# Performance work log

Measured on AMD Instinct MI355X. Metric: run time of the kernel, lower is better.

## Reference

```python
import jax, jax.numpy as jnp
import numpy as np

TAU = 2.0      # spikingjelly LIFNode default tau
V_TH = 1.0     # default v_threshold
ALPHA = 4.0    # default surrogate.Sigmoid alpha
H, HL = 8, 2   # num_heads, local_heads

@jax.custom_vjp
def spike(u):
    # Heaviside: fire when membrane potential >= threshold (u = v - v_th)
    return (u >= 0.0).astype(u.dtype)

def _spike_fwd(u):
    return spike(u), u

def _spike_bwd(u, g):
    s = jax.nn.sigmoid(ALPHA * u)
    return (g * ALPHA * s * (1.0 - s),)

spike.defvjp(_spike_fwd, _spike_bwd)

def lif(x):
    # Multi-step LIF, decay_input=False, v_reset=0.0 (hard reset), detach_reset=True.
    # Charge: v = v - (v - 0)/tau + x ; spike when v >= v_th ; reset v -> 0 where spiked.
    decay = 1.0 - 1.0 / TAU
    def step(v, xt):
        v = v * decay + xt
        s = spike(v - V_TH)
        v = v * (1.0 - jax.lax.stop_gradient(s))  # detach_reset
        return v, s
    _, spikes = jax.lax.scan(step, jnp.zeros_like(x[0]), x)
    return spikes

def setup_inputs() -> dict:
    key = jax.random.key(0)
    ks = jax.random.split(key, 5)
    T, B, C, D = 4, 8, 512, 768
    hd = D // H            # 96
    mkv = hd * HL          # 192 (GQA kv projection width)
    scale = 0.1            # keeps LIF membrane potentials near threshold
    return {
        "x": jax.random.normal(ks[0], (T, B, C, D), jnp.float32),
        "q_w": jax.random.normal(ks[1], (D, D), jnp.float32) * scale,
        "k_w": jax.random.normal(ks[2], (mkv, D), jnp.float32) * scale,
        "v_w": jax.random.normal(ks[3], (mkv, D), jnp.float32) * scale,
        "wo_w": jax.random.normal(ks[4], (D, D), jnp.float32) * scale,
    }

def reference(x, q_w, k_w, v_w, wo_w):
    T, B, C, D = x.shape
    hd = D // H
    n_rep = H // HL
    xs = lif(x)  # proj_lif
    # q: (T,B,C,D) -> (T,B,H,C,hd)
    q = lif(xs @ q_w.T).reshape(T, B, C, H, hd).transpose(0, 1, 3, 2, 4)
    # k,v: (T,B,C,mkv) -> repeat_interleave over kv heads -> (T,B,H,C,hd)
    k = lif(xs @ k_w.T).reshape(T, B, C, HL, hd)
    k = jnp.repeat(k, n_rep, axis=3).transpose(0, 1, 3, 2, 4)
    v = lif(xs @ v_w.T).reshape(T, B, C, HL, hd)
    v = jnp.repeat(v, n_rep, axis=3).transpose(0, 1, 3, 2, 4)
    # softmax-free attention: (q k^T) * 0.1 @ v
    scores = jnp.einsum('tbhqd,tbhkd->tbhqk', q, k) * 0.1
    out = jnp.einsum('tbhqk,tbhkd->tbhqd', scores, v)
    # (T,B,H,C,hd) -> (T,B,C,D)
    out = out.transpose(0, 1, 3, 2, 4).reshape(T, B, C, D)
    return out @ wo_w.T
```

## Files before the change

kernel.cpp:

```cpp
#include <hip/hip_runtime.h>

typedef __bf16 bf16;
typedef __bf16 bf16x8 __attribute__((ext_vector_type(8)));
typedef float f32x4 __attribute__((ext_vector_type(4)));

#define T_ 4
#define B_ 8
#define C_ 512
#define D_ 768
#define H_ 8
#define HL_ 2
#define HD_ 96
#define MKV_ 192
#define M2_ 4096
#define BCD_ 3145728
#define M3_ 16384
#define NCOMB 1152
#define SUSP_CAP 65536
#define SUSP_WIN 2e-4f

__device__ __forceinline__ void gld16(const bf16* g, bf16* l) {
    __builtin_amdgcn_global_load_lds(
        (const __attribute__((address_space(1))) unsigned int*)g,
        (__attribute__((address_space(3))) unsigned int*)l, 16, 0, 0);
}

__global__ __launch_bounds__(256) void prep_kernel(
    const float* __restrict__ x, const float* __restrict__ q_w,
    const float* __restrict__ k_w, const float* __restrict__ v_w,
    const float* __restrict__ wo_w, bf16* __restrict__ xs,
    bf16* __restrict__ whi, bf16* __restrict__ wlo, bf16* __restrict__ wo_bf,
    unsigned* __restrict__ susp)
{
    const int t0 = blockIdx.x * 256 + threadIdx.x;
    const int stride = gridDim.x * 256;
    if (t0 == 0) susp[0] = 0;
    for (int i = t0; i < BCD_; i += stride) {
        double v = 0.0;
        #pragma unroll
        for (int t = 0; t < T_; ++t) {
            v = v * 0.5 + (double)x[(size_t)t * BCD_ + i];
            float s = (v >= 1.0) ? 1.0f : 0.0f;
            xs[(size_t)t * BCD_ + i] = (bf16)s;
            if (s != 0.0f) v = 0.0;
        }
    }
    for (int i = t0; i < NCOMB * D_; i += stride) {
        int row = i / D_, col = i - row * D_;
        float v;
        if (row < 768)      v = q_w[(size_t)row * D_ + col];
        else if (row < 960) v = k_w[(size_t)(row - 768) * D_ + col];
        else                v = v_w[(size_t)(row - 960) * D_ + col];
        bf16 h = (bf16)v;
        whi[i] = h;
        wlo[i] = (bf16)(v - (float)h);
    }
    for (int i = t0; i < D_ * D_; i += stride)
        wo_bf[i] = (bf16)wo_w[i];
}

__global__ __launch_bounds__(256, 3) void proj_lif_kernel(
    const bf16* __restrict__ xs, const bf16* __restrict__ Whi,
    const bf16* __restrict__ Wlo,
    bf16* __restrict__ q_sp, bf16* __restrict__ k_sp, bf16* __restrict__ v_sp,
    unsigned* __restrict__ susp)
{
    __shared__ __align__(16) bf16 A0[T_][64 * 32];
    __shared__ __align__(16) bf16 A1[T_][64 * 32];
    __shared__ __align__(16) bf16 H0[64 * 32];
    __shared__ __align__(16) bf16 H1[64 * 32];
    __shared__ __align__(16) bf16 L0[64 * 32];
    __shared__ __align__(16) bf16 L1[64 * 32];

    const int tid  = threadIdx.x;
    const int wave = tid >> 6, lane = tid & 63;
    const int m16  = lane & 15, quad = lane >> 4;
    const int wm   = wave >> 1, wn = wave & 1;

    const int bid   = blockIdx.y * 64 + blockIdx.x;
    const int xcd   = bid & 7;
    const int local = bid >> 3;
    const int m0    = ((xcd << 3) | (local & 7)) * 64;
    const int n0    = (local >> 3) * 64;

    const int colb = n0 + wn * 32;
    bf16* outp; int Nloc, cb;
    if (colb < 768)      { outp = q_sp; Nloc = 768; cb = colb; }
    else if (colb < 960) { outp = k_sp; Nloc = 192; cb = colb - 768; }
    else                 { outp = v_sp; Nloc = 192; cb = colb - 960; }

    f32x4 acc[T_][2][2];
    #pragma unroll
    for (int t = 0; t < T_; t++)
        #pragma unroll
        for (int a = 0; a < 2; a++)
            #pragma unroll
            for (int b = 0; b < 2; b++) { f32x4 z = {0.f,0.f,0.f,0.f}; acc[t][a][b] = z; }

    const int srow = tid >> 2;
    const int sseg = (tid & 3) ^ ((tid >> 3) & 3);

#define STAGE(Ab, Hb, Lb, k0) do {                                            \
    _Pragma("unroll")                                                         \
    for (int t = 0; t < T_; t++)                                              \
        gld16(xs + (size_t)(t * M2_ + m0 + srow) * D_ + (k0) + sseg * 8,      \
              &Ab[t][tid * 8]);                                               \
    gld16(Whi + (size_t)(n0 + srow) * D_ + (k0) + sseg * 8, &Hb[tid * 8]);    \
    gld16(Wlo + (size_t)(n0 + srow) * D_ + (k0) + sseg * 8, &Lb[tid * 8]);    \
} while (0)

    bf16x8 a[T_][2], bh[2], bl[2];

#define LOADREGS(Ab, Hb, Lb) do {                                             \
    _Pragma("unroll")                                                         \
    for (int mi = 0; mi < 2; mi++) {                                          \
        int row = wm * 32 + mi * 16 + m16;                                    \
        int off = row * 32 + ((quad ^ ((row >> 1) & 3)) * 8);                 \
        _Pragma("unroll")                                                     \
        for (int t = 0; t < T_; t++) a[t][mi] = *(const bf16x8*)&Ab[t][off];  \
    }                                                                         \
    _Pragma("unroll")                                                         \
    for (int ni = 0; ni < 2; ni++) {                                          \
        int row = wn * 32 + ni * 16 + m16;                                    \
        int off = row * 32 + ((quad ^ ((row >> 1) & 3)) * 8);                 \
        bh[ni] = *(const bf16x8*)&Hb[off];                                    \
        bl[ni] = *(const bf16x8*)&Lb[off];                                    \
    }                                                                         \
} while (0)

#define DOMFMA() do {                                                         \
    __builtin_amdgcn_s_setprio(1);                                            \
    _Pragma("unroll")                                                         \
    for (int ni = 0; ni < 2; ni++)                                            \
        _Pragma("unroll")                                                     \
        for (int t = 0; t < T_; t++)                                          \
            _Pragma("unroll")                                                 \
            for (int mi = 0; mi < 2; mi++) {                                  \
                acc[t][mi][ni] = __builtin_amdgcn_mfma_f32_16x16x32_bf16(     \
                    a[t][mi], bh[ni], acc[t][mi][ni], 0, 0, 0);               \
                acc[t][mi][ni] = __builtin_amdgcn_mfma_f32_16x16x32_bf16(     \
                    a[t][mi], bl[ni], acc[t][mi][ni], 0, 0, 0);               \
            }                                                                 \
    __builtin_amdgcn_s_setprio(0);                                            \
} while (0)

#define READS_DONE() do {                                                     \
    asm volatile("s_waitcnt lgkmcnt(0)" ::: "memory");                        \
    __builtin_amdgcn_s_barrier();                                             \
    __builtin_amdgcn_sched_barrier(0);                                        \
} while (0)

#define NEXT_READY(N) do {                                                    \
    asm volatile("s_waitcnt vmcnt(" #N ")" ::: "memory");                     \
    __builtin_amdgcn_s_barrier();                                             \
} while (0)

    STAGE(A0, H0, L0, 0);
    STAGE(A1, H1, L1, 32);
    NEXT_READY(6);

    for (int s = 0; s < 22; s += 2) {
        LOADREGS(A0, H0, L0);
        READS_DONE();
        STAGE(A0, H0, L0, (s + 2) * 32);
        DOMFMA();
        NEXT_READY(6);

        LOADREGS(A1, H1, L1);
        READS_DONE();
        STAGE(A1, H1, L1, (s + 3) * 32);
        DOMFMA();
        NEXT_READY(6);
    }
    LOADREGS(A0, H0, L0);
    READS_DONE();
    DOMFMA();
    NEXT_READY(0);
    LOADREGS(A1, H1, L1);
    DOMFMA();

#undef STAGE
#undef LOADREGS
#undef DOMFMA
#undef READS_DONE
#undef NEXT_READY

    #pragma unroll
    for (int mi = 0; mi < 2; mi++)
        #pragma unroll
        for (int ni = 0; ni < 2; ni++)
            #pragma unroll
            for (int rr = 0; rr < 4; rr++) {
                int row = m0 + wm * 32 + mi * 16 + quad * 4 + rr;
                int lc  = cb + ni * 16 + m16;
                float v = 0.f;
                bool suspect = false;
                #pragma unroll
                for (int t = 0; t < T_; t++) {
                    v = v * 0.5f + acc[t][mi][ni][rr];
                    float d = v - 1.0f;
                    if (fabsf(d) < SUSP_WIN) suspect = true;
                    float sp = (d >= 0.f) ? 1.f : 0.f;
                    v *= (1.f - sp);
                    outp[(size_t)(t * M2_ + row) * Nloc + lc] = (bf16)sp;
                }
                if (suspect) {
                    int ccol = n0 + wn * 32 + ni * 16 + m16;
                    unsigned idx = atomicAdd(susp, 1u);
                    if (idx < SUSP_CAP) susp[1 + idx] = (unsigned)(row * 2048 + ccol);
                }
            }
}

__global__ __launch_bounds__(256) void fixup_kernel(
    const bf16* __restrict__ xs, const float* __restrict__ q_w,
    const float* __restrict__ k_w, const float* __restrict__ v_w,
    bf16* __restrict__ q_sp, bf16* __restrict__ k_sp, bf16* __restrict__ v_sp,
    const unsigned* __restrict__ susp)
{
    unsigned count = susp[0];
    if (count > SUSP_CAP) count = SUSP_CAP;
    const int lane = threadIdx.x & 63;
    const int wid  = (blockIdx.x * blockDim.x + threadIdx.x) >> 6;
    const int nw   = (gridDim.x * blockDim.x) >> 6;
    for (unsigned i = wid; i < count; i += nw) {
        unsigned e = susp[1 + i];
        int row = e >> 11, col = e & 2047;
        const float* W; bf16* outp; int Nloc, lc;
        if (col < 768)      { W = q_w + (size_t)col * D_;         outp = q_sp; Nloc = 768; lc = col; }
        else if (col < 960) { W = k_w + (size_t)(col - 768) * D_; outp = k_sp; Nloc = 192; lc = col - 768; }
        else                { W = v_w + (size_t)(col - 960) * D_; outp = v_sp; Nloc = 192; lc = col - 960; }
        double v = 0.0;
        for (int t = 0; t < T_; ++t) {
            const bf16* ar = xs + (size_t)(t * M2_ + row) * D_;
            double y = 0.0;
            for (int k = lane; k < D_; k += 64)
                y += (double)(float)ar[k] * (double)W[k];
            #pragma unroll
            for (int off = 1; off < 64; off <<= 1)
                y += __shfl_xor(y, off);
            v = v * 0.5 + y;
            unsigned sp = (v >= 1.0) ? 1u : 0u;
            if (lane == 0) outp[(size_t)(t * M2_ + row) * Nloc + lc] = (bf16)(float)sp;
            if (sp) v = 0.0;
        }
    }
}

__global__ __launch_bounds__(256) void ktv_kernel(
    const bf16* __restrict__ k_sp, const bf16* __restrict__ v_sp,
    float* __restrict__ M_part)
{
    const int g    = blockIdx.x;
    const int cc   = blockIdx.y;
    const int kvh  = g % HL_;
    const int tb   = g / HL_;
    const int wave = threadIdx.x >> 6;
    const int lane = threadIdx.x & 63;
    const int m16  = lane & 15, quad = lane >> 4;

    __shared__ __align__(16) bf16 klds[96 * 40];
    __shared__ __align__(16) bf16 vlds[96 * 40];

    f32x4 acc[9];
    #pragma unroll
    for (int i = 0; i < 9; i++) { f32x4 z = {0.f,0.f,0.f,0.f}; acc[i] = z; }

    const bf16* kbase = k_sp + ((size_t)tb * C_ + cc * 64) * MKV_ + kvh * HD_;
    const bf16* vbase = v_sp + ((size_t)tb * C_ + cc * 64) * MKV_ + kvh * HD_;

    for (int c0 = 0; c0 < 64; c0 += 32) {
        __syncthreads();
        for (int ci = threadIdx.x; ci < 768; ci += 256) {
            int arr = ci & 1;
            int pos = ci >> 1;
            int c = pos / 12, seg = pos - c * 12;
            const bf16* src = (arr ? vbase : kbase) + (size_t)(c0 + c) * MKV_ + seg * 8;
            bf16x8 val = *(const bf16x8*)src;
            bf16* dst = arr ? vlds : klds;
            #pragma unroll
            for (int e = 0; e < 8; e++)
                dst[(seg * 8 + e) * 40 + c] = val[e];
        }
        __syncthreads();
        #pragma unroll
        for (int i = 0; i < 9; i++) {
            int tile = wave + i * 4;
            int mt = tile / 6, nt = tile % 6;
            bf16x8 a = *(const bf16x8*)(&klds[(mt * 16 + m16) * 40 + quad * 8]);
            bf16x8 b = *(const bf16x8*)(&vlds[(nt * 16 + m16) * 40 + quad * 8]);
            acc[i] = __builtin_amdgcn_mfma_f32_16x16x32_bf16(a, b, acc[i], 0, 0, 0);
        }
    }
    float* op = M_part + ((size_t)cc * 64 + g) * HD_ * HD_;
    #pragma unroll
    for (int i = 0; i < 9; i++) {
        int tile = wave + i * 4;
        int mt = tile / 6, nt = tile % 6;
        #pragma unroll
        for (int r = 0; r < 4; r++) {
            int d = mt * 16 + quad * 4 + r;
            int j = nt * 16 + m16;
            op[(size_t)j * HD_ + d] = acc[i][r];
        }
    }
}

__global__ __launch_bounds__(256) void cvtM_kernel(
    const float* __restrict__ M_part, bf16* __restrict__ M_hi,
    bf16* __restrict__ M_lo)
{
    int i = blockIdx.x * 256 + threadIdx.x;
    if (i >= 64 * HD_ * HD_) return;
    float m = 0.f;
    #pragma unroll
    for (int j = 0; j < 8; j++)
        m += M_part[i + (size_t)j * 589824];
    bf16 h = (bf16)m;
    M_hi[i] = h;
    M_lo[i] = (bf16)(m - (float)h);
}

__global__ __launch_bounds__(256) void qm_kernel(
    const bf16* __restrict__ q_sp, const bf16* __restrict__ M_hi,
    const bf16* __restrict__ M_lo, bf16* __restrict__ out_attn)
{
    const int tbh  = blockIdx.x;
    const int h    = tbh % H_;
    const int tb   = tbh / H_;
    const int g    = tb * HL_ + (h >> 2);
    const int wave = threadIdx.x >> 6;
    const int lane = threadIdx.x & 63;
    const int m16  = lane & 15, quad = lane >> 4;
    const int cw   = blockIdx.y * 128 + wave * 32;

    __shared__ __align__(16) bf16 Mh[96 * 104];
    __shared__ __align__(16) bf16 Ml[96 * 104];
    {
        const bf16* gh = M_hi + (size_t)g * HD_ * HD_;
        const bf16* gl = M_lo + (size_t)g * HD_ * HD_;
        #pragma unroll
        for (int j = 0; j < 5; j++) {
            int ci = j * 256 + threadIdx.x;
            if (ci < 1152) {
                int row = ci / 12, seg = ci % 12;
                *(bf16x8*)&Mh[row * 104 + seg * 8] = *(const bf16x8*)(gh + row * HD_ + seg * 8);
                *(bf16x8*)&Ml[row * 104 + seg * 8] = *(const bf16x8*)(gl + row * HD_ + seg * 8);
            }
        }
    }
    __syncthreads();

    f32x4 acc[2][6];
    #pragma unroll
    for (int mi = 0; mi < 2; mi++)
        #pragma unroll
        for (int nt = 0; nt < 6; nt++) { f32x4 z = {0.f,0.f,0.f,0.f}; acc[mi][nt] = z; }

    #pragma unroll
    for (int ks = 0; ks < 3; ++ks) {
        bf16x8 a[2];
        #pragma unroll
        for (int mi = 0; mi < 2; mi++)
            a[mi] = *(const bf16x8*)(q_sp + ((size_t)(tb * C_ + cw + mi * 16 + m16)) * D_
                                     + h * HD_ + ks * 32 + quad * 8);
        #pragma unroll
        for (int nt = 0; nt < 6; ++nt) {
            bf16x8 bh = *(const bf16x8*)&Mh[(nt * 16 + m16) * 104 + ks * 32 + quad * 8];
            bf16x8 bl = *(const bf16x8*)&Ml[(nt * 16 + m16) * 104 + ks * 32 + quad * 8];
            #pragma unroll
            for (int mi = 0; mi < 2; mi++) {
                acc[mi][nt] = __builtin_amdgcn_mfma_f32_16x16x32_bf16(a[mi], bh, acc[mi][nt], 0, 0, 0);
                acc[mi][nt] = __builtin_amdgcn_mfma_f32_16x16x32_bf16(a[mi], bl, acc[mi][nt], 0, 0, 0);
            }
        }
    }
    #pragma unroll
    for (int mi = 0; mi < 2; mi++)
        #pragma unroll
        for (int nt = 0; nt < 6; nt++)
            #pragma unroll
            for (int r = 0; r < 4; r++) {
                int c = cw + mi * 16 + quad * 4 + r;
                int j = nt * 16 + m16;
                out_attn[((size_t)(tb * C_ + c)) * D_ + h * HD_ + j] = (bf16)(0.1f * acc[mi][nt][r]);
            }
}

__global__ __launch_bounds__(256) void final_gemm_kernel(
    const bf16* __restrict__ A, const bf16* __restrict__ W, float* __restrict__ out)
{
    __shared__ __align__(16) bf16 Alds[128 * 64];
    __shared__ __align__(16) bf16 Blds[128 * 64];
    const int tid  = threadIdx.x;
    const int wave = tid >> 6, lane = tid & 63;
    const int m16  = lane & 15, quad = lane >> 4;
    const int wm   = wave >> 1, wn = wave & 1;
    const int m0   = blockIdx.x * 128, n0 = blockIdx.y * 128;

    f32x4 acc[4][4];
    #pragma unroll
    for (int a = 0; a < 4; a++)
        #pragma unroll
        for (int b = 0; b < 4; b++) { f32x4 z = {0.f,0.f,0.f,0.f}; acc[a][b] = z; }

    for (int k0 = 0; k0 < D_; k0 += 64) {
        __syncthreads();
        #pragma unroll
        for (int j = 0; j < 4; j++) {
            int ci = j * 256 + tid;
            int row = ci >> 3, slot = ci & 7;
            int seg = slot ^ ((row >> 1) & 7);
            gld16(A + (size_t)(m0 + row) * D_ + k0 + seg * 8, Alds + ci * 8);
            gld16(W + (size_t)(n0 + row) * D_ + k0 + seg * 8, Blds + ci * 8);
        }
        __syncthreads();
        #pragma unroll
        for (int kc = 0; kc < 2; kc++) {
            bf16x8 a[4], b[4];
            #pragma unroll
            for (int mi = 0; mi < 4; mi++) {
                int row = wm * 64 + mi * 16 + m16;
                a[mi] = *(const bf16x8*)&Alds[row * 64 + (((kc * 4 + quad) ^ ((row >> 1) & 7)) * 8)];
            }
            #pragma unroll
            for (int ni = 0; ni < 4; ni++) {
                int row = wn * 64 + ni * 16 + m16;
                b[ni] = *(const bf16x8*)&Blds[row * 64 + (((kc * 4 + quad) ^ ((row >> 1) & 7)) * 8)];
            }
            #pragma unroll
            for (int mi = 0; mi < 4; mi++)
                #pragma unroll
                for (int ni = 0; ni < 4; ni++)
                    acc[mi][ni] = __builtin_amdgcn_mfma_f32_16x16x32_bf16(a[mi], b[ni], acc[mi][ni], 0, 0, 0);
        }
    }
    #pragma unroll
    for (int mi = 0; mi < 4; mi++)
        #pragma unroll
        for (int ni = 0; ni < 4; ni++)
            #pragma unroll
            for (int r = 0; r < 4; r++) {
                int row = m0 + wm * 64 + mi * 16 + quad * 4 + r;
                int col = n0 + wn * 64 + ni * 16 + m16;
                out[(size_t)row * D_ + col] = acc[mi][ni][r];
            }
}

extern "C" void kernel_launch(void* const* d_in, const int* in_sizes, int n_in,
                              void* d_out, int out_size, void* d_ws, size_t ws_size,
                              hipStream_t stream) {
    const float* x    = (const float*)d_in[0];
    const float* q_w  = (const float*)d_in[1];
    const float* k_w  = (const float*)d_in[2];
    const float* v_w  = (const float*)d_in[3];
    const float* wo_w = (const float*)d_in[4];
    float* out = (float*)d_out;

    char* ws = (char*)d_ws;
    bf16* xs    = (bf16*)(ws);
    bf16* q_sp  = (bf16*)(ws + 25165824);
    bf16* k_sp  = (bf16*)(ws + 50331648);
    bf16* v_sp  = (bf16*)(ws + 56623104);
    bf16* whi   = (bf16*)(ws + 62914560);
    bf16* wlo   = (bf16*)(ws + 64684032);
    bf16* wo_bf = (bf16*)(ws + 66453504);
    bf16* M_hi  = (bf16*)(ws + 67633152);
    bf16* M_lo  = (bf16*)(ws + 68812800);
    unsigned* susp = (unsigned*)(ws + 69992448);
    bf16* out_attn = xs;
    float* M_part  = out;

    hipLaunchKernelGGL(prep_kernel, dim3(2048), dim3(256), 0, stream,
                       x, q_w, k_w, v_w, wo_w, xs, whi, wlo, wo_bf, susp);
    hipLaunchKernelGGL(proj_lif_kernel, dim3(M2_ / 64, NCOMB / 64), dim3(256), 0, stream,
                       xs, whi, wlo, q_sp, k_sp, v_sp, susp);
    hipLaunchKernelGGL(fixup_kernel, dim3(256), dim3(256), 0, stream,
                       xs, q_w, k_w, v_w, q_sp, k_sp, v_sp, susp);
    hipLaunchKernelGGL(ktv_kernel, dim3(T_ * B_ * HL_, 8), dim3(256), 0, stream,
                       k_sp, v_sp, M_part);
    hipLaunchKernelGGL(cvtM_kernel, dim3((64 * HD_ * HD_ + 255) / 256), dim3(256), 0, stream,
                       M_part, M_hi, M_lo);
    hipLaunchKernelGGL(qm_kernel, dim3(T_ * B_ * H_, C_ / 128), dim3(256), 0, stream,
                       q_sp, M_hi, M_lo, out_attn);
    hipLaunchKernelGGL(final_gemm_kernel, dim3(M3_ / 128, D_ / 128), dim3(256), 0, stream,
                       out_attn, wo_bf, out);
}
```

Measured before the change: 266.0 us.

## Vectorize prep, fuse fixup into projection epilogue, double-buffer final GEMM

Prep now handles 8 elements of the LIF input scan and 4 elements of each weight conversion per thread, using vector loads and stores. The separate fixup kernel and its global atomic suspect list go away. Each projection wave instead ballots its near-threshold outputs and recomputes them in double precision in its own epilogue, which saves a launch but can serialize waves that hit many suspects. The final GEMM switches to double-buffered 32-wide K stages with explicit waitcnt and barrier pipelining and launch_bounds 3, so loads overlap MFMA work.

New measurement: 255.8 us. 1.04x faster.

```diff
diff --git a/kernel.cpp b/kernel.cpp
--- a/kernel.cpp
+++ b/kernel.cpp
@@ -1,6 +1,7 @@
 #include <hip/hip_runtime.h>
 
 typedef __bf16 bf16;
+typedef __bf16 bf16x4 __attribute__((ext_vector_type(4)));
 typedef __bf16 bf16x8 __attribute__((ext_vector_type(8)));
 typedef float f32x4 __attribute__((ext_vector_type(4)));
 
@@ -16,7 +17,6 @@
 #define BCD_ 3145728
 #define M3_ 16384
 #define NCOMB 1152
-#define SUSP_CAP 65536
 #define SUSP_WIN 2e-4f
 
 __device__ __forceinline__ void gld16(const bf16* g, bf16* l) {
@@ -25,45 +25,76 @@
         (__attribute__((address_space(3))) unsigned int*)l, 16, 0, 0);
 }
 
+#define READS_DONE() do {                                                     \
+    asm volatile("s_waitcnt lgkmcnt(0)" ::: "memory");                        \
+    __builtin_amdgcn_s_barrier();                                             \
+    __builtin_amdgcn_sched_barrier(0);                                        \
+} while (0)
+
+#define NEXT_READY(N) do {                                                    \
+    asm volatile("s_waitcnt vmcnt(" #N ")" ::: "memory");                     \
+    __builtin_amdgcn_s_barrier();                                             \
+} while (0)
+
 __global__ __launch_bounds__(256) void prep_kernel(
     const float* __restrict__ x, const float* __restrict__ q_w,
     const float* __restrict__ k_w, const float* __restrict__ v_w,
     const float* __restrict__ wo_w, bf16* __restrict__ xs,
-    bf16* __restrict__ whi, bf16* __restrict__ wlo, bf16* __restrict__ wo_bf,
-    unsigned* __restrict__ susp)
+    bf16* __restrict__ whi, bf16* __restrict__ wlo, bf16* __restrict__ wo_bf)
 {
     const int t0 = blockIdx.x * 256 + threadIdx.x;
     const int stride = gridDim.x * 256;
-    if (t0 == 0) susp[0] = 0;
-    for (int i = t0; i < BCD_; i += stride) {
-        double v = 0.0;
+    for (int i = t0 * 8; i < BCD_; i += stride * 8) {
+        double v[8] = {0.0, 0.0, 0.0, 0.0, 0.0, 0.0, 0.0, 0.0};
         #pragma unroll
         for (int t = 0; t < T_; ++t) {
-            v = v * 0.5 + (double)x[(size_t)t * BCD_ + i];
-            float s = (v >= 1.0) ? 1.0f : 0.0f;
-            xs[(size_t)t * BCD_ + i] = (bf16)s;
-            if (s != 0.0f) v = 0.0;
-        }
-    }
-    for (int i = t0; i < NCOMB * D_; i += stride) {
+            const float* xp = x + (size_t)t * BCD_ + i;
+            f32x4 xa = *(const f32x4*)xp;
+            f32x4 xb = *(const f32x4*)(xp + 4);
+            bf16x8 s;
+            #pragma unroll
+            for (int e = 0; e < 8; ++e) {
+                float xe = (e < 4) ? xa[e] : xb[e - 4];
+                v[e] = v[e] * 0.5 + (double)xe;
+                float sp = (v[e] >= 1.0) ? 1.f : 0.f;
+                s[e] = (bf16)sp;
+                v[e] *= (double)(1.f - sp);
+            }
+            *(bf16x8*)(xs + (size_t)t * BCD_ + i) = s;
+        }
+    }
+    for (int i = t0 * 4; i < NCOMB * D_; i += stride * 4) {
         int row = i / D_, col = i - row * D_;
-        float v;
-        if (row < 768)      v = q_w[(size_t)row * D_ + col];
-        else if (row < 960) v = k_w[(size_t)(row - 768) * D_ + col];
-        else                v = v_w[(size_t)(row - 960) * D_ + col];
-        bf16 h = (bf16)v;
-        whi[i] = h;
-        wlo[i] = (bf16)(v - (float)h);
-    }
-    for (int i = t0; i < D_ * D_; i += stride)
-        wo_bf[i] = (bf16)wo_w[i];
+        const float* src;
+        if (row < 768)      src = q_w + (size_t)row * D_ + col;
+        else if (row < 960) src = k_w + (size_t)(row - 768) * D_ + col;
+        else                src = v_w + (size_t)(row - 960) * D_ + col;
+        f32x4 wv = *(const f32x4*)src;
+        bf16x4 hh, ll;
+        #pragma unroll
+        for (int e = 0; e < 4; ++e) {
+            bf16 h = (bf16)wv[e];
+            hh[e] = h;
+            ll[e] = (bf16)(wv[e] - (float)h);
+        }
+        *(bf16x4*)(whi + i) = hh;
+        *(bf16x4*)(wlo + i) = ll;
+    }
+    for (int i = t0 * 4; i < D_ * D_; i += stride * 4) {
+        f32x4 wv = *(const f32x4*)(wo_w + i);
+        bf16x4 c;
+        #pragma unroll
+        for (int e = 0; e < 4; ++e) c[e] = (bf16)wv[e];
+        *(bf16x4*)(wo_bf + i) = c;
+    }
 }
 
 __global__ __launch_bounds__(256, 3) void proj_lif_kernel(
     const bf16* __restrict__ xs, const bf16* __restrict__ Whi,
     const bf16* __restrict__ Wlo,
-    bf16* __restrict__ q_sp, bf16* __restrict__ k_sp, bf16* __restrict__ v_sp,
-    unsigned* __restrict__ susp)
+    const float* __restrict__ q_w, const float* __restrict__ k_w,
+    const float* __restrict__ v_w,
+    bf16* __restrict__ q_sp, bf16* __restrict__ k_sp, bf16* __restrict__ v_sp)
 {
     __shared__ __align__(16) bf16 A0[T_][64 * 32];
     __shared__ __align__(16) bf16 A1[T_][64 * 32];
@@ -144,17 +175,6 @@
     __builtin_amdgcn_s_setprio(0);                                            \
 } while (0)
 
-#define READS_DONE() do {                                                     \
-    asm volatile("s_waitcnt lgkmcnt(0)" ::: "memory");                        \
-    __builtin_amdgcn_s_barrier();                                             \
-    __builtin_amdgcn_sched_barrier(0);                                        \
-} while (0)
-
-#define NEXT_READY(N) do {                                                    \
-    asm volatile("s_waitcnt vmcnt(" #N ")" ::: "memory");                     \
-    __builtin_amdgcn_s_barrier();                                             \
-} while (0)
-
     STAGE(A0, H0, L0, 0);
     STAGE(A1, H1, L1, 32);
     NEXT_READY(6);
@@ -182,9 +202,8 @@
 #undef STAGE
 #undef LOADREGS
 #undef DOMFMA
-#undef READS_DONE
-#undef NEXT_READY
-
+
+    unsigned susmask = 0;
     #pragma unroll
     for (int mi = 0; mi < 2; mi++)
         #pragma unroll
@@ -204,45 +223,38 @@
                     v *= (1.f - sp);
                     outp[(size_t)(t * M2_ + row) * Nloc + lc] = (bf16)sp;
                 }
-                if (suspect) {
-                    int ccol = n0 + wn * 32 + ni * 16 + m16;
-                    unsigned idx = atomicAdd(susp, 1u);
-                    if (idx < SUSP_CAP) susp[1 + idx] = (unsigned)(row * 2048 + ccol);
-                }
-            }
-}
-
-__global__ __launch_bounds__(256) void fixup_kernel(
-    const bf16* __restrict__ xs, const float* __restrict__ q_w,
-    const float* __restrict__ k_w, const float* __restrict__ v_w,
-    bf16* __restrict__ q_sp, bf16* __restrict__ k_sp, bf16* __restrict__ v_sp,
-    const unsigned* __restrict__ susp)
-{
-    unsigned count = susp[0];
-    if (count > SUSP_CAP) count = SUSP_CAP;
-    const int lane = threadIdx.x & 63;
-    const int wid  = (blockIdx.x * blockDim.x + threadIdx.x) >> 6;
-    const int nw   = (gridDim.x * blockDim.x) >> 6;
-    for (unsigned i = wid; i < count; i += nw) {
-        unsigned e = susp[1 + i];
-        int row = e >> 11, col = e & 2047;
-        const float* W; bf16* outp; int Nloc, lc;
-        if (col < 768)      { W = q_w + (size_t)col * D_;         outp = q_sp; Nloc = 768; lc = col; }
-        else if (col < 960) { W = k_w + (size_t)(col - 768) * D_; outp = k_sp; Nloc = 192; lc = col - 768; }
-        else                { W = v_w + (size_t)(col - 960) * D_; outp = v_sp; Nloc = 192; lc = col - 960; }
-        double v = 0.0;
-        for (int t = 0; t < T_; ++t) {
-            const bf16* ar = xs + (size_t)(t * M2_ + row) * D_;
-            double y = 0.0;
-            for (int k = lane; k < D_; k += 64)
-                y += (double)(float)ar[k] * (double)W[k];
-            #pragma unroll
-            for (int off = 1; off < 64; off <<= 1)
-                y += __shfl_xor(y, off);
-            v = v * 0.5 + y;
-            unsigned sp = (v >= 1.0) ? 1u : 0u;
-            if (lane == 0) outp[(size_t)(t * M2_ + row) * Nloc + lc] = (bf16)(float)sp;
-            if (sp) v = 0.0;
+                if (suspect) susmask |= 1u << (mi * 8 + ni * 4 + rr);
+            }
+
+    #pragma unroll 1
+    for (int b = 0; b < 16; ++b) {
+        unsigned long long mask = __ballot((susmask >> b) & 1u);
+        while (mask) {
+            int src = (int)__ffsll((long long)mask) - 1;
+            mask &= mask - 1;
+            int mi = b >> 3, ni = (b >> 2) & 1, rr = b & 3;
+            int grow = m0 + wm * 32 + mi * 16 + ((src >> 4) << 2) + rr;
+            int gc   = n0 + wn * 32 + ni * 16 + (src & 15);
+            const float* Wr;
+            if (gc < 768)      Wr = q_w + (size_t)gc * D_;
+            else if (gc < 960) Wr = k_w + (size_t)(gc - 768) * D_;
+            else               Wr = v_w + (size_t)(gc - 960) * D_;
+            int lc = cb + ni * 16 + (src & 15);
+            double v = 0.0;
+            for (int t = 0; t < T_; ++t) {
+                const bf16* ar = xs + (size_t)(t * M2_ + grow) * D_;
+                double y = 0.0;
+                for (int k = lane; k < D_; k += 64)
+                    y += (double)(float)ar[k] * (double)Wr[k];
+                #pragma unroll
+                for (int off = 1; off < 64; off <<= 1)
+                    y += __shfl_xor(y, off);
+                v = v * 0.5 + y;
+                float sp = (v >= 1.0) ? 1.f : 0.f;
+                if (lane == 0)
+                    outp[(size_t)(t * M2_ + grow) * Nloc + lc] = (bf16)sp;
+                if (sp != 0.f) v = 0.0;
+            }
         }
     }
 }
@@ -387,11 +399,14 @@
             }
 }
 
-__global__ __launch_bounds__(256) void final_gemm_kernel(
+__global__ __launch_bounds__(256, 3) void final_gemm_kernel(
     const bf16* __restrict__ A, const bf16* __restrict__ W, float* __restrict__ out)
 {
-    __shared__ __align__(16) bf16 Alds[128 * 64];
-    __shared__ __align__(16) bf16 Blds[128 * 64];
+    __shared__ __align__(16) bf16 FA0[128 * 32];
+    __shared__ __align__(16) bf16 FA1[128 * 32];
+    __shared__ __align__(16) bf16 FB0[128 * 32];
+    __shared__ __align__(16) bf16 FB1[128 * 32];
+
     const int tid  = threadIdx.x;
     const int wave = tid >> 6, lane = tid & 63;
     const int m16  = lane & 15, quad = lane >> 4;
@@ -400,41 +415,76 @@
 
     f32x4 acc[4][4];
     #pragma unroll
-    for (int a = 0; a < 4; a++)
-        #pragma unroll
-        for (int b = 0; b < 4; b++) { f32x4 z = {0.f,0.f,0.f,0.f}; acc[a][b] = z; }
-
-    for (int k0 = 0; k0 < D_; k0 += 64) {
-        __syncthreads();
-        #pragma unroll
-        for (int j = 0; j < 4; j++) {
-            int ci = j * 256 + tid;
-            int row = ci >> 3, slot = ci & 7;
-            int seg = slot ^ ((row >> 1) & 7);
-            gld16(A + (size_t)(m0 + row) * D_ + k0 + seg * 8, Alds + ci * 8);
-            gld16(W + (size_t)(n0 + row) * D_ + k0 + seg * 8, Blds + ci * 8);
-        }
-        __syncthreads();
-        #pragma unroll
-        for (int kc = 0; kc < 2; kc++) {
-            bf16x8 a[4], b[4];
-            #pragma unroll
-            for (int mi = 0; mi < 4; mi++) {
-                int row = wm * 64 + mi * 16 + m16;
-                a[mi] = *(const bf16x8*)&Alds[row * 64 + (((kc * 4 + quad) ^ ((row >> 1) & 7)) * 8)];
-            }
-            #pragma unroll
-            for (int ni = 0; ni < 4; ni++) {
-                int row = wn * 64 + ni * 16 + m16;
-                b[ni] = *(const bf16x8*)&Blds[row * 64 + (((kc * 4 + quad) ^ ((row >> 1) & 7)) * 8)];
-            }
-            #pragma unroll
-            for (int mi = 0; mi < 4; mi++)
-                #pragma unroll
-                for (int ni = 0; ni < 4; ni++)
-                    acc[mi][ni] = __builtin_amdgcn_mfma_f32_16x16x32_bf16(a[mi], b[ni], acc[mi][ni], 0, 0, 0);
-        }
-    }
+    for (int p = 0; p < 4; p++)
+        #pragma unroll
+        for (int q = 0; q < 4; q++) { f32x4 z = {0.f,0.f,0.f,0.f}; acc[p][q] = z; }
+
+    const int c0_ = tid,        r0_ = c0_ >> 2, g0_ = (c0_ & 3) ^ ((c0_ >> 3) & 3);
+    const int c1_ = 256 + tid,  r1_ = c1_ >> 2, g1_ = (c1_ & 3) ^ ((c1_ >> 3) & 3);
+
+#define FSTG(Ab, Bb, k0) do {                                                 \
+    gld16(A + (size_t)(m0 + r0_) * D_ + (k0) + g0_ * 8, &Ab[c0_ * 8]);        \
+    gld16(A + (size_t)(m0 + r1_) * D_ + (k0) + g1_ * 8, &Ab[c1_ * 8]);        \
+    gld16(W + (size_t)(n0 + r0_) * D_ + (k0) + g0_ * 8, &Bb[c0_ * 8]);        \
+    gld16(W + (size_t)(n0 + r1_) * D_ + (k0) + g1_ * 8, &Bb[c1_ * 8]);        \
+} while (0)
+
+    bf16x8 fa[4], fb[4];
+
+#define FLOAD(Ab, Bb) do {                                                    \
+    _Pragma("unroll")                                                         \
+    for (int mi = 0; mi < 4; mi++) {                                          \
+        int row = wm * 64 + mi * 16 + m16;                                    \
+        int off = row * 32 + ((quad ^ ((row >> 1) & 3)) * 8);                 \
+        fa[mi] = *(const bf16x8*)&Ab[off];                                    \
+    }                                                                         \
+    _Pragma("unroll")                                                         \
+    for (int ni = 0; ni < 4; ni++) {                                          \
+        int row = wn * 64 + ni * 16 + m16;                                    \
+        int off = row * 32 + ((quad ^ ((row >> 1) & 3)) * 8);                 \
+        fb[ni] = *(const bf16x8*)&Bb[off];                                    \
+    }                                                                         \
+} while (0)
+
+#define FMFMA() do {                                                          \
+    __builtin_amdgcn_s_setprio(1);                                            \
+    _Pragma("unroll")                                                         \
+    for (int mi = 0; mi < 4; mi++)                                            \
+        _Pragma("unroll")                                                     \
+        for (int ni = 0; ni < 4; ni++)                                        \
+            acc[mi][ni] = __builtin_amdgcn_mfma_f32_16x16x32_bf16(            \
+                fa[mi], fb[ni], acc[mi][ni], 0, 0, 0);                        \
+    __builtin_amdgcn_s_setprio(0);                                            \
+} while (0)
+
+    FSTG(FA0, FB0, 0);
+    FSTG(FA1, FB1, 32);
+    NEXT_READY(4);
+
+    for (int s = 0; s < 22; s += 2) {
+        FLOAD(FA0, FB0);
+        READS_DONE();
+        FSTG(FA0, FB0, (s + 2) * 32);
+        FMFMA();
+        NEXT_READY(4);
+
+        FLOAD(FA1, FB1);
+        READS_DONE();
+        FSTG(FA1, FB1, (s + 3) * 32);
+        FMFMA();
+        NEXT_READY(4);
+    }
+    FLOAD(FA0, FB0);
+    READS_DONE();
+    FMFMA();
+    NEXT_READY(0);
+    FLOAD(FA1, FB1);
+    FMFMA();
+
+#undef FSTG
+#undef FLOAD
+#undef FMFMA
+
     #pragma unroll
     for (int mi = 0; mi < 4; mi++)
         #pragma unroll
@@ -467,16 +517,13 @@
     bf16* wo_bf = (bf16*)(ws + 66453504);
     bf16* M_hi  = (bf16*)(ws + 67633152);
     bf16* M_lo  = (bf16*)(ws + 68812800);
-    unsigned* susp = (unsigned*)(ws + 69992448);
     bf16* out_attn = xs;
     float* M_part  = out;
 
-    hipLaunchKernelGGL(prep_kernel, dim3(2048), dim3(256), 0, stream,
-                       x, q_w, k_w, v_w, wo_w, xs, whi, wlo, wo_bf, susp);
+    hipLaunchKernelGGL(prep_kernel, dim3(1536), dim3(256), 0, stream,
+                       x, q_w, k_w, v_w, wo_w, xs, whi, wlo, wo_bf);
     hipLaunchKernelGGL(proj_lif_kernel, dim3(M2_ / 64, NCOMB / 64), dim3(256), 0, stream,
-                       xs, whi, wlo, q_sp, k_sp, v_sp, susp);
-    hipLaunchKernelGGL(fixup_kernel, dim3(256), dim3(256), 0, stream,
-                       xs, q_w, k_w, v_w, q_sp, k_sp, v_sp, susp);
+                       xs, whi, wlo, q_w, k_w, v_w, q_sp, k_sp, v_sp);
     hipLaunchKernelGGL(ktv_kernel, dim3(T_ * B_ * HL_, 8), dim3(256), 0, stream,
                        k_sp, v_sp, M_part);
     hipLaunchKernelGGL(cvtM_kernel, dim3((64 * HD_ * HD_ + 255) / 256), dim3(256), 0, stream,
```
